# Kernel tuning notes

Measured on AMD Instinct MI355X. Metric: run time of the kernel, lower is better.

## Reference

```python
import jax, jax.numpy as jnp
import numpy as np

B, C, P = 32, 192, 3136
EPS = 0.01


def setup_inputs() -> dict:
    key = jax.random.key(0)
    k1, k2, k3 = jax.random.split(key, 3)
    return {
        "embeddings": jax.random.normal(k1, (B, C, P), dtype=jnp.float32),
        "means": jax.random.normal(k2, (P, C), dtype=jnp.float32),
        "covariances": jax.random.normal(k3, (P, C, C), dtype=jnp.float32),
        "n": 96,
    }


def reference(embeddings, means, covariances, n):
    # embeddings: [B, C, P]; means: [P, C] (running sums); covariances: [P, C, C] (running outer-product sums)
    b = embeddings.shape[0]
    c = embeddings.shape[1]
    # Training-branch accumulation: per-patch sum of outer products over the batch,
    # expressed as one batched GEMM instead of P*B tiny torch.outer calls.
    new_means = means + jnp.einsum("bcp->pc", embeddings)
    new_covs = covariances + jnp.einsum("bcp,bdp->pcd", embeddings, embeddings)
    n_new = n + b
    # calculate_means_and_covariances(): finalize sample mean / covariance per patch.
    learned_means = new_means / n_new  # [P, C]
    learned_covs = (new_covs - n_new * jnp.einsum("pc,pd->pcd", learned_means, learned_means)) / (n_new - 1)
    learned_covs = learned_covs + EPS * jnp.eye(c, dtype=learned_covs.dtype)
    return (learned_means, learned_covs)
```

## Files before the change

kernel.cpp:

```cpp
#include <hip/hip_runtime.h>


#define BB 32
#define CC 192
#define PP 3136
#define EPSV 0.01f

__global__ __launch_bounds__(256) void padim_kernel(
    const float* __restrict__ emb,
    const float* __restrict__ means,
    const float* __restrict__ covs,
    const int*   __restrict__ n_ptr,
    float* __restrict__ out_means,
    float* __restrict__ out_covs)
{
    __shared__ __align__(16) float E[BB][CC + 4];
    __shared__ __align__(16) float m[CC];

    const int bid = blockIdx.x;
    const int p = (bid & 7) * (PP / 8) + (bid >> 3);

    const int t = threadIdx.x;

    const float n_new = (float)(n_ptr[0] + BB);
    const float inv_nnew = 1.0f / n_new;
    const float inv_nm1 = 1.0f / (n_new - 1.0f);

    #pragma unroll
    for (int i = t; i < BB * CC; i += 256) {
        const int b = i / CC;
        const int c = i - b * CC;
        E[b][c] = emb[(size_t)i * PP + p];
    }
    __syncthreads();

    if (t < CC) {
        float s = 0.0f;
        #pragma unroll
        for (int b = 0; b < BB; ++b) s += E[b][t];
        const float mm = (means[(size_t)p * CC + t] + s) * inv_nnew;
        m[t] = mm;
        out_means[(size_t)p * CC + t] = mm;
    }
    __syncthreads();

    const int tx = t & 15;
    const int ty = t >> 4;
    const float* __restrict__ cov_p = covs + (size_t)p * CC * CC;
    float* __restrict__ out_p = out_covs + (size_t)p * CC * CC;

    #pragma unroll 1
    for (int pass = 0; pass < 9; ++pass) {
        const int tc = pass / 3;
        const int td = pass - tc * 3;
        const int c0 = tc * 64 + ty * 4;
        const int d0 = td * 64 + tx * 4;

        float acc[4][4] = {{0.f,0.f,0.f,0.f},{0.f,0.f,0.f,0.f},
                           {0.f,0.f,0.f,0.f},{0.f,0.f,0.f,0.f}};

        #pragma unroll 8
        for (int b = 0; b < BB; ++b) {
            const float4 cv = *reinterpret_cast<const float4*>(&E[b][c0]);
            const float4 dv = *reinterpret_cast<const float4*>(&E[b][d0]);
            const float cs[4] = {cv.x, cv.y, cv.z, cv.w};
            const float ds[4] = {dv.x, dv.y, dv.z, dv.w};
            #pragma unroll
            for (int i = 0; i < 4; ++i)
                #pragma unroll
                for (int j = 0; j < 4; ++j)
                    acc[i][j] = fmaf(cs[i], ds[j], acc[i][j]);
        }

        const float4 mc4 = *reinterpret_cast<const float4*>(&m[c0]);
        const float4 md4 = *reinterpret_cast<const float4*>(&m[d0]);
        const float mcs[4] = {mc4.x, mc4.y, mc4.z, mc4.w};
        const float mds[4] = {md4.x, md4.y, md4.z, md4.w};

        #pragma unroll
        for (int i = 0; i < 4; ++i) {
            const int c = c0 + i;
            const size_t row = (size_t)c * CC + d0;
            const float4 cin = *reinterpret_cast<const float4*>(&cov_p[row]);
            const float nm_c = n_new * mcs[i];
            float4 o;
            o.x = (cin.x + acc[i][0] - nm_c * mds[0]) * inv_nm1;
            o.y = (cin.y + acc[i][1] - nm_c * mds[1]) * inv_nm1;
            o.z = (cin.z + acc[i][2] - nm_c * mds[2]) * inv_nm1;
            o.w = (cin.w + acc[i][3] - nm_c * mds[3]) * inv_nm1;
            if (c == d0 + 0) o.x += EPSV;
            if (c == d0 + 1) o.y += EPSV;
            if (c == d0 + 2) o.z += EPSV;
            if (c == d0 + 3) o.w += EPSV;
            *reinterpret_cast<float4*>(&out_p[row]) = o;
        }
    }
}

extern "C" void kernel_launch(void* const* d_in, const int* in_sizes, int n_in,
                              void* d_out, int out_size, void* d_ws, size_t ws_size,
                              hipStream_t stream) {
    const float* emb   = (const float*)d_in[0];
    const float* means = (const float*)d_in[1];
    const float* covs  = (const float*)d_in[2];
    const int*   n_ptr = (const int*)d_in[3];

    float* out_means = (float*)d_out;
    float* out_covs  = (float*)d_out + (size_t)PP * CC;

    hipLaunchKernelGGL(padim_kernel, dim3(PP), dim3(256), 0, stream,
                       emb, means, covs, n_ptr, out_means, out_covs);
}
```

Measured before the change: 254.3 us.

## Compute full 192x192 covariance tile per block with 12x12 register micro-tiles

Replaces nine passes of 4x4 outer-product tiles with a single pass in which each thread accumulates a 12x12 register tile over the batch. Each shared-memory read of E now feeds more FMAs, and the pass loop overhead goes away. It also removes the padding on the shared E array and requests two blocks per CU through launch bounds. The cost is about 144 accumulators per thread, which raises register pressure and may cause spills. Global cov reads and writes become strided 48-byte chunks per thread rather than contiguous rows, which can hurt coalescing in what is largely a memory-bound kernel.

```diff
diff --git a/kernel.cpp b/kernel.cpp
--- a/kernel.cpp
+++ b/kernel.cpp
@@ -6,7 +6,7 @@
 #define PP 3136
 #define EPSV 0.01f
 
-__global__ __launch_bounds__(256) void padim_kernel(
+__global__ __launch_bounds__(256, 2) void padim_kernel(
     const float* __restrict__ emb,
     const float* __restrict__ means,
     const float* __restrict__ covs,
@@ -14,12 +14,11 @@
     float* __restrict__ out_means,
     float* __restrict__ out_covs)
 {
-    __shared__ __align__(16) float E[BB][CC + 4];
+    __shared__ __align__(16) float E[BB][CC];
     __shared__ __align__(16) float m[CC];
 
     const int bid = blockIdx.x;
     const int p = (bid & 7) * (PP / 8) + (bid >> 3);
-
     const int t = threadIdx.x;
 
     const float n_new = (float)(n_ptr[0] + BB);
@@ -46,54 +45,79 @@
 
     const int tx = t & 15;
     const int ty = t >> 4;
+    const int c0 = ty * 12;
+    const int d0 = tx * 12;
+
+    float acc[12][12];
+    #pragma unroll
+    for (int i = 0; i < 12; ++i)
+        #pragma unroll
+        for (int j = 0; j < 12; ++j) acc[i][j] = 0.f;
+
+    #pragma unroll 2
+    for (int b = 0; b < BB; ++b) {
+        float cs[12], ds[12];
+        *reinterpret_cast<float4*>(&cs[0]) = *reinterpret_cast<const float4*>(&E[b][c0]);
+        *reinterpret_cast<float4*>(&cs[4]) = *reinterpret_cast<const float4*>(&E[b][c0 + 4]);
+        *reinterpret_cast<float4*>(&cs[8]) = *reinterpret_cast<const float4*>(&E[b][c0 + 8]);
+        *reinterpret_cast<float4*>(&ds[0]) = *reinterpret_cast<const float4*>(&E[b][d0]);
+        *reinterpret_cast<float4*>(&ds[4]) = *reinterpret_cast<const float4*>(&E[b][d0 + 4]);
+        *reinterpret_cast<float4*>(&ds[8]) = *reinterpret_cast<const float4*>(&E[b][d0 + 8]);
+        #pragma unroll
+        for (int i = 0; i < 12; ++i)
+            #pragma unroll
+            for (int j = 0; j < 12; ++j)
+                acc[i][j] = fmaf(cs[i], ds[j], acc[i][j]);
+    }
+
+    float mc[12], md[12];
+    *reinterpret_cast<float4*>(&mc[0]) = *reinterpret_cast<const float4*>(&m[c0]);
+    *reinterpret_cast<float4*>(&mc[4]) = *reinterpret_cast<const float4*>(&m[c0 + 4]);
+    *reinterpret_cast<float4*>(&mc[8]) = *reinterpret_cast<const float4*>(&m[c0 + 8]);
+    *reinterpret_cast<float4*>(&md[0]) = *reinterpret_cast<const float4*>(&m[d0]);
+    *reinterpret_cast<float4*>(&md[4]) = *reinterpret_cast<const float4*>(&m[d0 + 4]);
+    *reinterpret_cast<float4*>(&md[8]) = *reinterpret_cast<const float4*>(&m[d0 + 8]);
+
     const float* __restrict__ cov_p = covs + (size_t)p * CC * CC;
     float* __restrict__ out_p = out_covs + (size_t)p * CC * CC;
 
-    #pragma unroll 1
-    for (int pass = 0; pass < 9; ++pass) {
-        const int tc = pass / 3;
-        const int td = pass - tc * 3;
-        const int c0 = tc * 64 + ty * 4;
-        const int d0 = td * 64 + tx * 4;
-
-        float acc[4][4] = {{0.f,0.f,0.f,0.f},{0.f,0.f,0.f,0.f},
-                           {0.f,0.f,0.f,0.f},{0.f,0.f,0.f,0.f}};
-
-        #pragma unroll 8
-        for (int b = 0; b < BB; ++b) {
-            const float4 cv = *reinterpret_cast<const float4*>(&E[b][c0]);
-            const float4 dv = *reinterpret_cast<const float4*>(&E[b][d0]);
-            const float cs[4] = {cv.x, cv.y, cv.z, cv.w};
-            const float ds[4] = {dv.x, dv.y, dv.z, dv.w};
-            #pragma unroll
-            for (int i = 0; i < 4; ++i)
-                #pragma unroll
-                for (int j = 0; j < 4; ++j)
-                    acc[i][j] = fmaf(cs[i], ds[j], acc[i][j]);
+    #pragma unroll
+    for (int i = 0; i < 12; ++i) {
+        const size_t row = (size_t)(c0 + i) * CC + d0;
+        const float4 cin0 = *reinterpret_cast<const float4*>(&cov_p[row]);
+        const float4 cin1 = *reinterpret_cast<const float4*>(&cov_p[row + 4]);
+        const float4 cin2 = *reinterpret_cast<const float4*>(&cov_p[row + 8]);
+        const float nmc = n_new * mc[i];
+        float4 o0, o1, o2;
+        o0.x = (cin0.x + acc[i][0]  - nmc * md[0])  * inv_nm1;
+        o0.y = (cin0.y + acc[i][1]  - nmc * md[1])  * inv_nm1;
+        o0.z = (cin0.z + acc[i][2]  - nmc * md[2])  * inv_nm1;
+        o0.w = (cin0.w + acc[i][3]  - nmc * md[3])  * inv_nm1;
+        o1.x = (cin1.x + acc[i][4]  - nmc * md[4])  * inv_nm1;
+        o1.y = (cin1.y + acc[i][5]  - nmc * md[5])  * inv_nm1;
+        o1.z = (cin1.z + acc[i][6]  - nmc * md[6])  * inv_nm1;
+        o1.w = (cin1.w + acc[i][7]  - nmc * md[7])  * inv_nm1;
+        o2.x = (cin2.x + acc[i][8]  - nmc * md[8])  * inv_nm1;
+        o2.y = (cin2.y + acc[i][9]  - nmc * md[9])  * inv_nm1;
+        o2.z = (cin2.z + acc[i][10] - nmc * md[10]) * inv_nm1;
+        o2.w = (cin2.w + acc[i][11] - nmc * md[11]) * inv_nm1;
+        if (tx == ty) {
+            if (i == 0)  o0.x += EPSV;
+            if (i == 1)  o0.y += EPSV;
+            if (i == 2)  o0.z += EPSV;
+            if (i == 3)  o0.w += EPSV;
+            if (i == 4)  o1.x += EPSV;
+            if (i == 5)  o1.y += EPSV;
+            if (i == 6)  o1.z += EPSV;
+            if (i == 7)  o1.w += EPSV;
+            if (i == 8)  o2.x += EPSV;
+            if (i == 9)  o2.y += EPSV;
+            if (i == 10) o2.z += EPSV;
+            if (i == 11) o2.w += EPSV;
         }
-
-        const float4 mc4 = *reinterpret_cast<const float4*>(&m[c0]);
-        const float4 md4 = *reinterpret_cast<const float4*>(&m[d0]);
-        const float mcs[4] = {mc4.x, mc4.y, mc4.z, mc4.w};
-        const float mds[4] = {md4.x, md4.y, md4.z, md4.w};
-
-        #pragma unroll
-        for (int i = 0; i < 4; ++i) {
-            const int c = c0 + i;
-            const size_t row = (size_t)c * CC + d0;
-            const float4 cin = *reinterpret_cast<const float4*>(&cov_p[row]);
-            const float nm_c = n_new * mcs[i];
-            float4 o;
-            o.x = (cin.x + acc[i][0] - nm_c * mds[0]) * inv_nm1;
-            o.y = (cin.y + acc[i][1] - nm_c * mds[1]) * inv_nm1;
-            o.z = (cin.z + acc[i][2] - nm_c * mds[2]) * inv_nm1;
-            o.w = (cin.w + acc[i][3] - nm_c * mds[3]) * inv_nm1;
-            if (c == d0 + 0) o.x += EPSV;
-            if (c == d0 + 1) o.y += EPSV;
-            if (c == d0 + 2) o.z += EPSV;
-            if (c == d0 + 3) o.w += EPSV;
-            *reinterpret_cast<float4*>(&out_p[row]) = o;
-        }
+        *reinterpret_cast<float4*>(&out_p[row])     = o0;
+        *reinterpret_cast<float4*>(&out_p[row + 4]) = o1;
+        *reinterpret_cast<float4*>(&out_p[row + 8]) = o2;
     }
 }
 
```

After: 337.9 us. +32.9%, slower.

## Enlarge per-thread register tile to 6x12 and cut covariance passes to two

Applied to the files above, without the earlier changes.

Replaces the nine 4x4 outer-product passes with two passes, each computing a 6x12 tile per thread. This raises FMA-to-LDS-load reuse in the batch reduction. It also removes the shared-memory row padding, hoists the d-side means into registers and adds a minimum-blocks hint of 3 to launch_bounds. The larger accumulator tile raises register pressure, which could cause spills or lower occupancy. The kernel is likely bound by streaming the covariance matrix from HBM anyway.

```diff
diff --git a/kernel.cpp b/kernel.cpp
--- a/kernel.cpp
+++ b/kernel.cpp
@@ -6,7 +6,7 @@
 #define PP 3136
 #define EPSV 0.01f
 
-__global__ __launch_bounds__(256) void padim_kernel(
+__global__ __launch_bounds__(256, 3) void padim_kernel(
     const float* __restrict__ emb,
     const float* __restrict__ means,
     const float* __restrict__ covs,
@@ -14,12 +14,11 @@
     float* __restrict__ out_means,
     float* __restrict__ out_covs)
 {
-    __shared__ __align__(16) float E[BB][CC + 4];
+    __shared__ __align__(16) float E[BB][CC];
     __shared__ __align__(16) float m[CC];
 
     const int bid = blockIdx.x;
     const int p = (bid & 7) * (PP / 8) + (bid >> 3);
-
     const int t = threadIdx.x;
 
     const float n_new = (float)(n_ptr[0] + BB);
@@ -27,7 +26,8 @@
     const float inv_nm1 = 1.0f / (n_new - 1.0f);
 
     #pragma unroll
-    for (int i = t; i < BB * CC; i += 256) {
+    for (int k = 0; k < (BB * CC) / 256; ++k) {
+        const int i = t + k * 256;
         const int b = i / CC;
         const int c = i - b * CC;
         E[b][c] = emb[(size_t)i * PP + p];
@@ -46,53 +46,68 @@
 
     const int tx = t & 15;
     const int ty = t >> 4;
+    const int dbase0 = tx * 4;
+
     const float* __restrict__ cov_p = covs + (size_t)p * CC * CC;
     float* __restrict__ out_p = out_covs + (size_t)p * CC * CC;
 
-    #pragma unroll 1
-    for (int pass = 0; pass < 9; ++pass) {
-        const int tc = pass / 3;
-        const int td = pass - tc * 3;
-        const int c0 = tc * 64 + ty * 4;
-        const int d0 = td * 64 + tx * 4;
+    float md[12];
+    *reinterpret_cast<float4*>(&md[0]) = *reinterpret_cast<const float4*>(&m[dbase0]);
+    *reinterpret_cast<float4*>(&md[4]) = *reinterpret_cast<const float4*>(&m[64 + dbase0]);
+    *reinterpret_cast<float4*>(&md[8]) = *reinterpret_cast<const float4*>(&m[128 + dbase0]);
 
-        float acc[4][4] = {{0.f,0.f,0.f,0.f},{0.f,0.f,0.f,0.f},
-                           {0.f,0.f,0.f,0.f},{0.f,0.f,0.f,0.f}};
+    #pragma unroll
+    for (int pass = 0; pass < 2; ++pass) {
+        const int c0 = pass * 96 + ty * 6;
 
-        #pragma unroll 8
+        float acc[6][12];
+        #pragma unroll
+        for (int i = 0; i < 6; ++i)
+            #pragma unroll
+            for (int j = 0; j < 12; ++j) acc[i][j] = 0.f;
+
+        #pragma unroll 4
         for (int b = 0; b < BB; ++b) {
-            const float4 cv = *reinterpret_cast<const float4*>(&E[b][c0]);
-            const float4 dv = *reinterpret_cast<const float4*>(&E[b][d0]);
-            const float cs[4] = {cv.x, cv.y, cv.z, cv.w};
-            const float ds[4] = {dv.x, dv.y, dv.z, dv.w};
+            float cs[6], ds[12];
+            *reinterpret_cast<float4*>(&ds[0]) = *reinterpret_cast<const float4*>(&E[b][dbase0]);
+            *reinterpret_cast<float4*>(&ds[4]) = *reinterpret_cast<const float4*>(&E[b][64 + dbase0]);
+            *reinterpret_cast<float4*>(&ds[8]) = *reinterpret_cast<const float4*>(&E[b][128 + dbase0]);
+            *reinterpret_cast<float2*>(&cs[0]) = *reinterpret_cast<const float2*>(&E[b][c0]);
+            *reinterpret_cast<float2*>(&cs[2]) = *reinterpret_cast<const float2*>(&E[b][c0 + 2]);
+            *reinterpret_cast<float2*>(&cs[4]) = *reinterpret_cast<const float2*>(&E[b][c0 + 4]);
             #pragma unroll
-            for (int i = 0; i < 4; ++i)
+            for (int i = 0; i < 6; ++i)
                 #pragma unroll
-                for (int j = 0; j < 4; ++j)
+                for (int j = 0; j < 12; ++j)
                     acc[i][j] = fmaf(cs[i], ds[j], acc[i][j]);
         }
 
-        const float4 mc4 = *reinterpret_cast<const float4*>(&m[c0]);
-        const float4 md4 = *reinterpret_cast<const float4*>(&m[d0]);
-        const float mcs[4] = {mc4.x, mc4.y, mc4.z, mc4.w};
-        const float mds[4] = {md4.x, md4.y, md4.z, md4.w};
+        float mc[6];
+        *reinterpret_cast<float2*>(&mc[0]) = *reinterpret_cast<const float2*>(&m[c0]);
+        *reinterpret_cast<float2*>(&mc[2]) = *reinterpret_cast<const float2*>(&m[c0 + 2]);
+        *reinterpret_cast<float2*>(&mc[4]) = *reinterpret_cast<const float2*>(&m[c0 + 4]);
 
         #pragma unroll
-        for (int i = 0; i < 4; ++i) {
+        for (int i = 0; i < 6; ++i) {
             const int c = c0 + i;
-            const size_t row = (size_t)c * CC + d0;
-            const float4 cin = *reinterpret_cast<const float4*>(&cov_p[row]);
-            const float nm_c = n_new * mcs[i];
-            float4 o;
-            o.x = (cin.x + acc[i][0] - nm_c * mds[0]) * inv_nm1;
-            o.y = (cin.y + acc[i][1] - nm_c * mds[1]) * inv_nm1;
-            o.z = (cin.z + acc[i][2] - nm_c * mds[2]) * inv_nm1;
-            o.w = (cin.w + acc[i][3] - nm_c * mds[3]) * inv_nm1;
-            if (c == d0 + 0) o.x += EPSV;
-            if (c == d0 + 1) o.y += EPSV;
-            if (c == d0 + 2) o.z += EPSV;
-            if (c == d0 + 3) o.w += EPSV;
-            *reinterpret_cast<float4*>(&out_p[row]) = o;
+            const size_t row = (size_t)c * CC;
+            const float nmc = n_new * mc[i];
+            #pragma unroll
+            for (int g = 0; g < 3; ++g) {
+                const int db = g * 64 + dbase0;
+                const float4 cin = *reinterpret_cast<const float4*>(&cov_p[row + db]);
+                float4 o;
+                o.x = (cin.x + acc[i][g*4+0] - nmc * md[g*4+0]) * inv_nm1;
+                o.y = (cin.y + acc[i][g*4+1] - nmc * md[g*4+1]) * inv_nm1;
+                o.z = (cin.z + acc[i][g*4+2] - nmc * md[g*4+2]) * inv_nm1;
+                o.w = (cin.w + acc[i][g*4+3] - nmc * md[g*4+3]) * inv_nm1;
+                const int dd = c - db;
+                if (dd == 0) o.x += EPSV;
+                if (dd == 1) o.y += EPSV;
+                if (dd == 2) o.z += EPSV;
+                if (dd == 3) o.w += EPSV;
+                *reinterpret_cast<float4*>(&out_p[row + db]) = o;
+            }
         }
     }
 }
```

New measurement: 252.7 us. About the same (-0.6%).
